# Kernel optimization log

Measured on AMD Instinct MI355X. Metric: run time of the kernel, lower is better.

Reference implementation:

```python
import jax, jax.numpy as jnp
from jax import lax
import numpy as np

B, T, M, AUX, H, OUT = 256, 256, 8, 32, 64, 1

def setup_inputs() -> dict:
    key = jax.random.key(0)
    ks = jax.random.split(key, 12)
    s_aux = 1.0 / np.sqrt(AUX)
    s_h = 1.0 / np.sqrt(H)
    return {
        "x_m": jax.random.uniform(ks[0], (B, T, M), dtype=jnp.float32),
        "x_a": jax.random.normal(ks[1], (B, T, AUX), dtype=jnp.float32),
        # junction: aux -> (M, H) logits, softmax over H (outgoing mass fractions)
        "Wj": jax.random.uniform(ks[2], (AUX, M * H), jnp.float32, -s_aux, s_aux),
        "bj": jnp.zeros((M * H,), jnp.float32),
        # redistribution: aux -> (H, H) logits, softmax over last dim
        "Wr": jax.random.uniform(ks[3], (AUX, H * H), jnp.float32, -s_aux, s_aux),
        "br": jnp.zeros((H * H,), jnp.float32),
        # out gate: sigmoid(Linear(aux))
        "Wo": jax.random.uniform(ks[4], (AUX, H), jnp.float32, -s_aux, s_aux),
        "bo": jnp.zeros((H,), jnp.float32),
        # final fc: hidden -> out_size
        "Wfc": jax.random.uniform(ks[5], (H, OUT), jnp.float32, -s_h, s_h),
        "bfc": jnp.zeros((OUT,), jnp.float32),
    }


def reference(x_m, x_a, Wj, bj, Wr, br, Wo, bo, Wfc, bfc):
    Bb = x_m.shape[0]

    def step(c, xs):
        xm, xa = xs  # [B, M], [B, AUX]
        j = jax.nn.softmax((xa @ Wj + bj).reshape(Bb, M, H), axis=-1)
        r = jax.nn.softmax((xa @ Wr + br).reshape(Bb, H, H), axis=-1)
        o = jax.nn.sigmoid(xa @ Wo + bo)
        m_in = jnp.einsum('bm,bmh->bh', xm, j)   # inflow distributed to cells
        m_sys = jnp.einsum('bh,bhk->bk', c, r)   # internal redistribution
        m_new = m_in + m_sys
        return m_new, o * m_new                  # (new cell state, output)

    c0 = jnp.zeros((Bb, H), dtype=x_m.dtype)
    xs = (jnp.swapaxes(x_m, 0, 1), jnp.swapaxes(x_a, 0, 1))  # time-major
    c_final, a = lax.scan(step, c0, xs)          # a: [T, B, H]
    out = a[-1] @ Wfc + bfc                      # fc on last timestep output
    return out, c_final
```

## Files before the change

### kernel.cpp

```cpp
#include <hip/hip_runtime.h>


namespace {

constexpr int B_ = 256, T_ = 256, M_ = 8, AUX_ = 32, H_ = 64;
constexpr int NTILE = 288;
constexpr float LOG2E = 1.4426950408889634f;

typedef __fp16 f16x2 __attribute__((ext_vector_type(2)));
typedef __fp16 f16x8 __attribute__((ext_vector_type(8)));
typedef float  f32x4 __attribute__((ext_vector_type(4)));
typedef int    i32x4 __attribute__((ext_vector_type(4)));

union V8 { f16x8 v; f16x2 p[4]; i32x4 i; };

#if __has_builtin(__builtin_amdgcn_exp2f)
#define EXP2(x) __builtin_amdgcn_exp2f(x)
#else
#define EXP2(x) exp2f(x)
#endif

template <int CTRL>
__device__ __forceinline__ float dpp_add(float v) {
    int t = __builtin_amdgcn_update_dpp(0, __builtin_bit_cast(int, v),
                                        CTRL, 0xf, 0xf, true);
    return v + __builtin_bit_cast(float, t);
}
__device__ __forceinline__ float sum16_all(float v) {
    v = dpp_add<0xB1>(v);
    v = dpp_add<0x4E>(v);
    v = dpp_add<0x141>(v);
    v = dpp_add<0x140>(v);
    return v;
}
__device__ __forceinline__ float sum64_uni(float v) {
    v = dpp_add<0x111>(v); v = dpp_add<0x112>(v); v = dpp_add<0x114>(v);
    v = dpp_add<0x118>(v); v = dpp_add<0x142>(v); v = dpp_add<0x143>(v);
    return __builtin_bit_cast(float,
        __builtin_amdgcn_readlane(__builtin_bit_cast(int, v), 63));
}

#define LDS_FENCE() __asm__ volatile("s_waitcnt lgkmcnt(0)" ::: "memory")
#define C_FENCE()   __asm__ volatile("" ::: "memory")

__global__ __launch_bounds__(64)
void nomc_prep(const float* __restrict__ Wj, const float* __restrict__ bj,
               const float* __restrict__ Wr, const float* __restrict__ br,
               void* __restrict__ ws)
{
    const int gt = blockIdx.x;
    const int l = threadIdx.x, q = l >> 4, l15 = l & 15;
    const float* src; const float* bsrc; int stride;
    if (gt < 256) { const int n = gt * 16 + l15;        src = Wr + n; bsrc = br + n; stride = 4096; }
    else          { const int n = (gt - 256) * 16 + l15; src = Wj + n; bsrc = bj + n; stride = 512; }
    V8 v;
#pragma unroll
    for (int j = 0; j < 4; ++j) {
        const float f0 = src[(q * 8 + 2 * j)     * stride] * LOG2E;
        const float f1 = src[(q * 8 + 2 * j + 1) * stride] * LOG2E;
        v.p[j] = __builtin_amdgcn_cvt_pkrtz(f0, f1);
    }
    *(i32x4*)((char*)ws + (size_t)gt * 1024 + l * 16) = v.i;
    if (l < 16)
        ((float*)((char*)ws + NTILE * 1024))[gt * 16 + l] = bsrc[0] * LOG2E;
}

__global__ __launch_bounds__(1024, 4)
void nomc_main(const float* __restrict__ x_m, const float* __restrict__ x_a,
               const float* __restrict__ Wo, const float* __restrict__ bo,
               const float* __restrict__ Wfc, const float* __restrict__ bfc,
               const void* __restrict__ ws, float* __restrict__ out)
{
    const int b = blockIdx.x, tid = threadIdx.x;
    const int w = tid >> 6, l = tid & 63, q = l >> 4, l15 = l & 15;

    __shared__ __align__(16) __fp16 RT[16][8][64][8];
    __shared__ __align__(16) __fp16 JT[16][64][8];
    __shared__ float sinv[16][64];
    __shared__ __align__(16) __fp16 xj[16][32];
    __shared__ float xm_lds[T_][M_];
    __shared__ __align__(16) __fp16 cbuf[64];
    __shared__ float cfin_lds[H_];

    {
        const float* xmb = x_m + (size_t)b * T_ * M_;
        for (int i = tid; i < T_ * M_; i += 1024) (&xm_lds[0][0])[i] = xmb[i];
        for (int i = tid; i < 16 * 32; i += 1024) (&xj[0][0])[i] = (__fp16)0.f;
    }
    __syncthreads();

    const int ngrp = (w < 8) ? 5 : 4;
    const int g0   = (w < 8) ? w * 5 : 40 + (w - 8) * 4;
    const char* wsb = (const char*)ws;
    const float* wbias = (const float*)(wsb + NTILE * 1024);

    float c0 = 0.f, c1 = 0.f, c2 = 0.f, c3 = 0.f;

    for (int it = 0; it < 16; ++it) {
        V8 af;
        {
            const float* xa = x_a + ((size_t)b * T_ + it * 16 + l15) * AUX_ + q * 8;
            const f32x4 x0 = *(const f32x4*)xa;
            const f32x4 x1 = *(const f32x4*)(xa + 4);
            af.p[0] = __builtin_amdgcn_cvt_pkrtz(x0.x, x0.y);
            af.p[1] = __builtin_amdgcn_cvt_pkrtz(x0.z, x0.w);
            af.p[2] = __builtin_amdgcn_cvt_pkrtz(x1.x, x1.y);
            af.p[3] = __builtin_amdgcn_cvt_pkrtz(x1.z, x1.w);
        }

        for (int g = 0; g < ngrp; ++g) {
            const int gg = g0 + g;
            float es0 = 0.f, es1 = 0.f, es2 = 0.f, es3 = 0.f;
#pragma unroll
            for (int tt = 0; tt < 4; ++tt) {
                const int gt = gg * 4 + tt;
                V8 bf; bf.i = *(const i32x4*)(wsb + (size_t)gt * 1024 + l * 16);
                const float bv = wbias[gt * 16 + l15];
                f32x4 acc = {bv, bv, bv, bv};
                acc = __builtin_amdgcn_mfma_f32_16x16x32_f16(af.v, bf.v, acc, 0, 0, 0);
                const float e0 = EXP2(acc[0]), e1 = EXP2(acc[1]);
                const float e2 = EXP2(acc[2]), e3 = EXP2(acc[3]);
                const int kk = (tt << 4) + l15;
                if (gg < 64) {
                    const int hb = gg >> 3, p = gg & 7;
                    RT[q * 4 + 0][hb][kk][p] = (__fp16)e0;
                    RT[q * 4 + 1][hb][kk][p] = (__fp16)e1;
                    RT[q * 4 + 2][hb][kk][p] = (__fp16)e2;
                    RT[q * 4 + 3][hb][kk][p] = (__fp16)e3;
                } else {
                    const int mp = gg - 64;
                    JT[q * 4 + 0][kk][mp] = (__fp16)e0;
                    JT[q * 4 + 1][kk][mp] = (__fp16)e1;
                    JT[q * 4 + 2][kk][mp] = (__fp16)e2;
                    JT[q * 4 + 3][kk][mp] = (__fp16)e3;
                }
                es0 += e0; es1 += e1; es2 += e2; es3 += e3;
            }
            const float sr0 = sum16_all(es0), sr1 = sum16_all(es1);
            const float sr2 = sum16_all(es2), sr3 = sum16_all(es3);
            if (l15 == 0) {
                if (gg < 64) {
                    sinv[q * 4 + 0][gg] = __builtin_amdgcn_rcpf(sr0);
                    sinv[q * 4 + 1][gg] = __builtin_amdgcn_rcpf(sr1);
                    sinv[q * 4 + 2][gg] = __builtin_amdgcn_rcpf(sr2);
                    sinv[q * 4 + 3][gg] = __builtin_amdgcn_rcpf(sr3);
                } else {
                    const int m = gg - 64;
                    xj[q * 4 + 0][m] = (__fp16)(xm_lds[it * 16 + q * 4 + 0][m] * __builtin_amdgcn_rcpf(sr0));
                    xj[q * 4 + 1][m] = (__fp16)(xm_lds[it * 16 + q * 4 + 1][m] * __builtin_amdgcn_rcpf(sr1));
                    xj[q * 4 + 2][m] = (__fp16)(xm_lds[it * 16 + q * 4 + 2][m] * __builtin_amdgcn_rcpf(sr2));
                    xj[q * 4 + 3][m] = (__fp16)(xm_lds[it * 16 + q * 4 + 3][m] * __builtin_amdgcn_rcpf(sr3));
                }
            }
        }
        __syncthreads();

        if (w == 15) {
            for (int u = 0; u < 16; ++u) {
                const float cown = (q == 0) ? c0 : (q == 1) ? c1 : (q == 2) ? c2 : c3;
                cbuf[l] = (__fp16)(cown * sinv[u][l]);
                LDS_FENCE();
                V8 xjA; xjA.v = *(const f16x8*)&xj[u][q * 8];
                V8 A0;  A0.v  = *(const f16x8*)&cbuf[q * 8];
                V8 A1;  A1.v  = *(const f16x8*)&cbuf[32 + q * 8];
                float cn0, cn1, cn2, cn3;
#pragma unroll
                for (int kt = 0; kt < 4; ++kt) {
                    const int k = kt * 16 + l15;
                    V8 jB; jB.v = *(const f16x8*)&JT[u][k][0];
                    V8 b0; b0.v = *(const f16x8*)&RT[u][q][k][0];
                    V8 b1; b1.v = *(const f16x8*)&RT[u][4 + q][k][0];
                    f32x4 acc = {0.f, 0.f, 0.f, 0.f};
                    acc = __builtin_amdgcn_mfma_f32_16x16x32_f16(xjA.v, jB.v, acc, 0, 0, 0);
                    acc = __builtin_amdgcn_mfma_f32_16x16x32_f16(A0.v,  b0.v, acc, 0, 0, 0);
                    acc = __builtin_amdgcn_mfma_f32_16x16x32_f16(A1.v,  b1.v, acc, 0, 0, 0);
                    const float cv = acc[0];
                    if (kt == 0) cn0 = cv; else if (kt == 1) cn1 = cv;
                    else if (kt == 2) cn2 = cv; else cn3 = cv;
                }
                c0 = cn0; c1 = cn1; c2 = cn2; c3 = cn3;
                C_FENCE();
            }
        }
        __syncthreads();
    }

    if (w == 15) {
        const float cown = (q == 0) ? c0 : (q == 1) ? c1 : (q == 2) ? c2 : c3;
        cfin_lds[l] = cown;
        LDS_FENCE();
        const float* xa = x_a + ((size_t)b * T_ + (T_ - 1)) * AUX_;
        float L = bo[l];
#pragma unroll
        for (int a = 0; a < AUX_; ++a) L = fmaf(xa[a], Wo[a * H_ + l], L);
        const float o = 1.0f / (1.0f + __expf(-L));
        const float cfin = cfin_lds[l];
        float p = (o * cfin) * Wfc[l];
        p = sum64_uni(p);
        if (l == 0) out[b] = p + bfc[0];
        out[B_ + b * H_ + l] = cfin;
    }
}

}

extern "C" void kernel_launch(void* const* d_in, const int* in_sizes, int n_in,
                              void* d_out, int out_size, void* d_ws, size_t ws_size,
                              hipStream_t stream) {
    const float* x_m = (const float*)d_in[0];
    const float* x_a = (const float*)d_in[1];
    const float* Wj  = (const float*)d_in[2];
    const float* bj  = (const float*)d_in[3];
    const float* Wr  = (const float*)d_in[4];
    const float* br  = (const float*)d_in[5];
    const float* Wo  = (const float*)d_in[6];
    const float* bo  = (const float*)d_in[7];
    const float* Wfc = (const float*)d_in[8];
    const float* bfc = (const float*)d_in[9];
    float* out = (float*)d_out;

    hipLaunchKernelGGL(nomc_prep, dim3(NTILE), dim3(64), 0, stream,
                       Wj, bj, Wr, br, d_ws);
    hipLaunchKernelGGL(nomc_main, dim3(B_), dim3(1024), 0, stream,
                       x_m, x_a, Wo, bo, Wfc, bfc, d_ws, out);
}
```

Before: 265.8 us.

## Fuse weight prep into main kernel and XOR-swizzle LDS slot layout

Removes the separate prep kernel launch. Each block now converts its wave's slice of Wr/Wj to scaled fp16 tiles in the workspace itself and reads the biases directly from global memory. All 256 blocks write the same workspace data redundantly, and each wave only reads tiles it wrote, after a vmcnt fence. It also XOR-permutes the slot index for RT/JT/xj/cbuf so the stores and the matching K-ordered reads line up while reducing LDS bank conflicts. The trade is one fewer launch and dependency against redundant global traffic in every block.

Result: slower. 317.7 us (+19.5%).

```diff
diff --git a/kernel.cpp b/kernel.cpp
--- a/kernel.cpp
+++ b/kernel.cpp
@@ -4,7 +4,6 @@
 namespace {
 
 constexpr int B_ = 256, T_ = 256, M_ = 8, AUX_ = 32, H_ = 64;
-constexpr int NTILE = 288;
 constexpr float LOG2E = 1.4426950408889634f;
 
 typedef __fp16 f16x2 __attribute__((ext_vector_type(2)));
@@ -40,36 +39,17 @@
         __builtin_amdgcn_readlane(__builtin_bit_cast(int, v), 63));
 }
 
-#define LDS_FENCE() __asm__ volatile("s_waitcnt lgkmcnt(0)" ::: "memory")
-#define C_FENCE()   __asm__ volatile("" ::: "memory")
-
-__global__ __launch_bounds__(64)
-void nomc_prep(const float* __restrict__ Wj, const float* __restrict__ bj,
-               const float* __restrict__ Wr, const float* __restrict__ br,
-               void* __restrict__ ws)
-{
-    const int gt = blockIdx.x;
-    const int l = threadIdx.x, q = l >> 4, l15 = l & 15;
-    const float* src; const float* bsrc; int stride;
-    if (gt < 256) { const int n = gt * 16 + l15;        src = Wr + n; bsrc = br + n; stride = 4096; }
-    else          { const int n = (gt - 256) * 16 + l15; src = Wj + n; bsrc = bj + n; stride = 512; }
-    V8 v;
-#pragma unroll
-    for (int j = 0; j < 4; ++j) {
-        const float f0 = src[(q * 8 + 2 * j)     * stride] * LOG2E;
-        const float f1 = src[(q * 8 + 2 * j + 1) * stride] * LOG2E;
-        v.p[j] = __builtin_amdgcn_cvt_pkrtz(f0, f1);
-    }
-    *(i32x4*)((char*)ws + (size_t)gt * 1024 + l * 16) = v.i;
-    if (l < 16)
-        ((float*)((char*)ws + NTILE * 1024))[gt * 16 + l] = bsrc[0] * LOG2E;
-}
+#define LDS_FENCE()  __asm__ volatile("s_waitcnt lgkmcnt(0)" ::: "memory")
+#define VMEM_FENCE() __asm__ volatile("s_waitcnt vmcnt(0)" ::: "memory")
+#define C_FENCE()    __asm__ volatile("" ::: "memory")
 
 __global__ __launch_bounds__(1024, 4)
 void nomc_main(const float* __restrict__ x_m, const float* __restrict__ x_a,
+               const float* __restrict__ Wj, const float* __restrict__ bj,
+               const float* __restrict__ Wr, const float* __restrict__ br,
                const float* __restrict__ Wo, const float* __restrict__ bo,
                const float* __restrict__ Wfc, const float* __restrict__ bfc,
-               const void* __restrict__ ws, float* __restrict__ out)
+               void* ws, float* __restrict__ out)
 {
     const int b = blockIdx.x, tid = threadIdx.x;
     const int w = tid >> 6, l = tid & 63, q = l >> 4, l15 = l & 15;
@@ -82,6 +62,27 @@
     __shared__ __align__(16) __fp16 cbuf[64];
     __shared__ float cfin_lds[H_];
 
+    const int ngrp = (w < 8) ? 5 : 4;
+    const int g0   = (w < 8) ? w * 5 : 40 + (w - 8) * 4;
+    char* wsb = (char*)ws;
+
+    for (int c = 0; c < ngrp * 4; ++c) {
+        const int gt = g0 * 4 + c;
+        const int n = gt * 16 + l15;
+        const float* src; int stride;
+        if (gt < 256) { src = Wr + n;          stride = 4096; }
+        else          { src = Wj + (n - 4096); stride = 512;  }
+        V8 v;
+#pragma unroll
+        for (int j = 0; j < 4; ++j) {
+            const float f0 = src[(q * 8 + 2 * j)     * stride] * LOG2E;
+            const float f1 = src[(q * 8 + 2 * j + 1) * stride] * LOG2E;
+            v.p[j] = __builtin_amdgcn_cvt_pkrtz(f0, f1);
+        }
+        *(i32x4*)(wsb + (size_t)gt * 1024 + l * 16) = v.i;
+    }
+    VMEM_FENCE();
+
     {
         const float* xmb = x_m + (size_t)b * T_ * M_;
         for (int i = tid; i < T_ * M_; i += 1024) (&xm_lds[0][0])[i] = xmb[i];
@@ -89,10 +90,7 @@
     }
     __syncthreads();
 
-    const int ngrp = (w < 8) ? 5 : 4;
-    const int g0   = (w < 8) ? w * 5 : 40 + (w - 8) * 4;
-    const char* wsb = (const char*)ws;
-    const float* wbias = (const float*)(wsb + NTILE * 1024);
+    const int swq = q << 1;
 
     float c0 = 0.f, c1 = 0.f, c2 = 0.f, c3 = 0.f;
 
@@ -115,20 +113,21 @@
             for (int tt = 0; tt < 4; ++tt) {
                 const int gt = gg * 4 + tt;
                 V8 bf; bf.i = *(const i32x4*)(wsb + (size_t)gt * 1024 + l * 16);
-                const float bv = wbias[gt * 16 + l15];
+                const int n = gt * 16 + l15;
+                const float bv = ((gt < 256) ? br[n] : bj[n - 4096]) * LOG2E;
                 f32x4 acc = {bv, bv, bv, bv};
                 acc = __builtin_amdgcn_mfma_f32_16x16x32_f16(af.v, bf.v, acc, 0, 0, 0);
                 const float e0 = EXP2(acc[0]), e1 = EXP2(acc[1]);
                 const float e2 = EXP2(acc[2]), e3 = EXP2(acc[3]);
                 const int kk = (tt << 4) + l15;
                 if (gg < 64) {
-                    const int hb = gg >> 3, p = gg & 7;
+                    const int hb = gg >> 3, p = (gg & 7) ^ swq;
                     RT[q * 4 + 0][hb][kk][p] = (__fp16)e0;
                     RT[q * 4 + 1][hb][kk][p] = (__fp16)e1;
                     RT[q * 4 + 2][hb][kk][p] = (__fp16)e2;
                     RT[q * 4 + 3][hb][kk][p] = (__fp16)e3;
                 } else {
-                    const int mp = gg - 64;
+                    const int mp = (gg - 64) ^ swq;
                     JT[q * 4 + 0][kk][mp] = (__fp16)e0;
                     JT[q * 4 + 1][kk][mp] = (__fp16)e1;
                     JT[q * 4 + 2][kk][mp] = (__fp16)e2;
@@ -145,11 +144,11 @@
                     sinv[q * 4 + 2][gg] = __builtin_amdgcn_rcpf(sr2);
                     sinv[q * 4 + 3][gg] = __builtin_amdgcn_rcpf(sr3);
                 } else {
-                    const int m = gg - 64;
-                    xj[q * 4 + 0][m] = (__fp16)(xm_lds[it * 16 + q * 4 + 0][m] * __builtin_amdgcn_rcpf(sr0));
-                    xj[q * 4 + 1][m] = (__fp16)(xm_lds[it * 16 + q * 4 + 1][m] * __builtin_amdgcn_rcpf(sr1));
-                    xj[q * 4 + 2][m] = (__fp16)(xm_lds[it * 16 + q * 4 + 2][m] * __builtin_amdgcn_rcpf(sr2));
-                    xj[q * 4 + 3][m] = (__fp16)(xm_lds[it * 16 + q * 4 + 3][m] * __builtin_amdgcn_rcpf(sr3));
+                    const int m = gg - 64, mp = m ^ swq;
+                    xj[q * 4 + 0][mp] = (__fp16)(xm_lds[it * 16 + q * 4 + 0][m] * __builtin_amdgcn_rcpf(sr0));
+                    xj[q * 4 + 1][mp] = (__fp16)(xm_lds[it * 16 + q * 4 + 1][m] * __builtin_amdgcn_rcpf(sr1));
+                    xj[q * 4 + 2][mp] = (__fp16)(xm_lds[it * 16 + q * 4 + 2][m] * __builtin_amdgcn_rcpf(sr2));
+                    xj[q * 4 + 3][mp] = (__fp16)(xm_lds[it * 16 + q * 4 + 3][m] * __builtin_amdgcn_rcpf(sr3));
                 }
             }
         }
@@ -157,8 +156,9 @@
 
         if (w == 15) {
             for (int u = 0; u < 16; ++u) {
+                const int Xu = ((u >> 2) & 3) << 1;
                 const float cown = (q == 0) ? c0 : (q == 1) ? c1 : (q == 2) ? c2 : c3;
-                cbuf[l] = (__fp16)(cown * sinv[u][l]);
+                cbuf[(l & ~7) | ((l & 7) ^ Xu)] = (__fp16)(cown * sinv[u][l]);
                 LDS_FENCE();
                 V8 xjA; xjA.v = *(const f16x8*)&xj[u][q * 8];
                 V8 A0;  A0.v  = *(const f16x8*)&cbuf[q * 8];
@@ -219,8 +219,6 @@
     const float* bfc = (const float*)d_in[9];
     float* out = (float*)d_out;
 
-    hipLaunchKernelGGL(nomc_prep, dim3(NTILE), dim3(64), 0, stream,
-                       Wj, bj, Wr, br, d_ws);
     hipLaunchKernelGGL(nomc_main, dim3(B_), dim3(1024), 0, stream,
-                       x_m, x_a, Wo, bo, Wfc, bfc, d_ws, out);
-}
+                       x_m, x_a, Wj, bj, Wr, br, Wo, bo, Wfc, bfc, d_ws, out);
+}
```
